# Kernel tuning notes

Hardware: AMD Instinct MI355X
Metric: run time of the kernel (lower is better)

## Reference

```python
import jax, jax.numpy as jnp
from jax import lax
import numpy as np

IN_CH, OUT_CH, K, STRIDE = 4, 256, 16, 8
D_STATE, D_CONV, EXPAND, HEADDIM = 128, 4, 2, 64
D_INNER = EXPAND * OUT_CH            # 512
NHEADS = D_INNER // HEADDIM          # 8
CONV_DIM = D_INNER + 2 * D_STATE     # 768 (ngroups=1)
D_IN_PROJ = 2 * D_INNER + 2 * D_STATE + NHEADS  # 1288
B_SZ, L = 8, 16384


def _conv1d(x, w, b, stride, padding):
    y = lax.conv_general_dilated(x, w, (stride,), padding,
                                 dimension_numbers=('NCH', 'OIH', 'NCH'))
    return y + b[None, :, None]


def _mamba2(u, in_proj_w, conv1d_w, conv1d_b, dt_bias, A_log, D_skip, norm_w, out_proj_w):
    # u: (b, l, d_model). Faithful Mamba2 forward (ngroups=1, rmsnorm gated, no biases on projections).
    b, l, _ = u.shape
    zxbcdt = jnp.einsum('bld,ed->ble', u, in_proj_w)           # (b, l, d_in_proj)
    z = zxbcdt[..., :D_INNER]
    xBC = zxbcdt[..., D_INNER:D_INNER + CONV_DIM]
    dt = jax.nn.softplus(zxbcdt[..., D_INNER + CONV_DIM:] + dt_bias)  # (b, l, h)
    # causal depthwise conv (torch pads d_conv-1 both sides then truncates to :l == left-pad only) + SiLU
    xBC = lax.conv_general_dilated(xBC.transpose(0, 2, 1), conv1d_w, (1,),
                                   [(D_CONV - 1, 0)], feature_group_count=CONV_DIM,
                                   dimension_numbers=('NCH', 'OIH', 'NCH'))
    xBC = jax.nn.silu((xBC + conv1d_b[None, :, None]).transpose(0, 2, 1))  # (b, l, conv_dim)
    xs = xBC[..., :D_INNER].reshape(b, l, NHEADS, HEADDIM)
    Bm = xBC[..., D_INNER:D_INNER + D_STATE]                   # (b, l, n)
    Cm = xBC[..., D_INNER + D_STATE:]                          # (b, l, n)
    A = -jnp.exp(A_log)                                        # (h,), scalar A per head
    dA = jnp.exp(dt * A)                                       # (b, l, h)

    def step(h, inp):
        dA_t, dt_t, x_t, B_t, C_t = inp
        h = h * dA_t[:, :, None, None] + jnp.einsum('bh,bhp,bn->bhpn', dt_t, x_t, B_t)
        return h, jnp.einsum('bhpn,bn->bhp', h, C_t)

    h0 = jnp.zeros((b, NHEADS, HEADDIM, D_STATE), dtype=u.dtype)
    _, ys = lax.scan(step, h0, (dA.swapaxes(0, 1), dt.swapaxes(0, 1),
                                xs.swapaxes(0, 1), Bm.swapaxes(0, 1), Cm.swapaxes(0, 1)))
    y = ys.swapaxes(0, 1) + D_skip[None, None, :, None] * xs   # (b, l, h, p)
    y = y.reshape(b, l, D_INNER) * jax.nn.silu(z)              # gated RMSNorm (norm_before_gate=False)
    y = y * lax.rsqrt(jnp.mean(y * y, axis=-1, keepdims=True) + 1e-5) * norm_w
    return jnp.einsum('ble,de->bld', y, out_proj_w)


def _forward(x, conv_w, conv_b, in_proj_w, conv1d_w, conv1d_b, dt_bias, A_log,
             D_skip, norm_w, out_proj_w, conv1_w, conv1_b, convT_w, convT_b):
    h = jax.nn.relu(_conv1d(x, conv_w, conv_b, STRIDE, 'VALID'))       # (b, out_ch, l')
    y = _mamba2(h.transpose(0, 2, 1), in_proj_w, conv1d_w, conv1d_b,
                dt_bias, A_log, D_skip, norm_w, out_proj_w)
    y = y.transpose(0, 2, 1)                                           # (b, out_ch, l')
    y = _conv1d(y, conv1_w, conv1_b, 1, [(7, 8)])  # torch padding='same', even kernel: left=7, right=8
    # ConvTranspose1d: torch weight (Cin, Cout, K) -> flipped OIH kernel + lhs dilation
    kern = jnp.flip(convT_w, -1).transpose(1, 0, 2)
    y = lax.conv_general_dilated(y, kern, (1,), [(K - 1, K - 1)], lhs_dilation=(STRIDE,),
                                 dimension_numbers=('NCH', 'OIH', 'NCH'))
    return y + convT_b[None, :, None]


def setup_inputs() -> dict:
    key = jax.random.key(0)
    ks = jax.random.split(key, 16)
    n = lambda k, shp, sc=0.05: jax.random.normal(k, shp, dtype=jnp.float32) * sc
    return {
        'x': jax.random.normal(ks[0], (B_SZ, IN_CH, L), dtype=jnp.float32),
        'conv_w': n(ks[1], (OUT_CH, IN_CH, K)),
        'conv_b': n(ks[2], (OUT_CH,)),
        'in_proj_w': n(ks[3], (D_IN_PROJ, OUT_CH)),
        'conv1d_w': n(ks[4], (CONV_DIM, 1, D_CONV), 0.3),
        'conv1d_b': n(ks[5], (CONV_DIM,), 0.1),
        'dt_bias': n(ks[6], (NHEADS,), 0.5),
        'A_log': jnp.log(jax.random.uniform(ks[7], (NHEADS,), minval=1.0, maxval=16.0)),
        'D_skip': n(ks[8], (NHEADS,), 1.0),
        'norm_w': jnp.ones((D_INNER,), dtype=jnp.float32),
        'out_proj_w': n(ks[9], (OUT_CH, D_INNER)),
        'conv1_w': n(ks[10], (STRIDE, OUT_CH, K)),
        'conv1_b': n(ks[11], (STRIDE,)),
        'convT_w': n(ks[12], (STRIDE, IN_CH, K)),
        'convT_b': n(ks[13], (IN_CH,)),
    }


def reference(x, conv_w, conv_b, in_proj_w, conv1d_w, conv1d_b, dt_bias, A_log,
              D_skip, norm_w, out_proj_w, conv1_w, conv1_b, convT_w, convT_b):
    return _forward(x, conv_w, conv_b, in_proj_w, conv1d_w, conv1d_b, dt_bias, A_log,
                    D_skip, norm_w, out_proj_w, conv1_w, conv1_b, convT_w, convT_b)
```

## Files before the change

### kernel.cpp

```cpp
#include <hip/hip_runtime.h>
#include <cstddef>
#include <cstdint>

constexpr int L_IN   = 16384;
constexpr int L_SEQ  = 2047;
constexpr int BATCH  = 8;
constexpr int M_TOK  = BATCH * L_SEQ;
constexpr int D_INNER = 512;
constexpr int NHEADS  = 8;
constexpr int HEADDIM = 64;
constexpr int D_STATE = 128;
constexpr int CONV_DIM = 768;
constexpr int D_IN_PROJ = 1288;

constexpr int QC  = 64;
constexpr int NCH = 32;

constexpr size_t OFF_U    = 0;
constexpr size_t OFF_PB   = OFF_U   + 2096128;
constexpr size_t OFF_ZB   = OFF_U   + 4192256;
constexpr size_t OFF_XBC  = OFF_ZB  + 4192256;
constexpr size_t OFF_DT   = OFF_XBC + 6288384;
constexpr size_t OFF_AW   = OFF_DT  + 131008;
constexpr size_t OFF_XC   = OFF_AW  + 131008;
constexpr size_t OFF_Y    = OFF_XC  + 6288384;
constexpr size_t OFF_YC1  = OFF_Y   + 4192256;
constexpr size_t OFF_PBUF = OFF_YC1 + 131008;
constexpr size_t OFF_HS   = OFF_PBUF + 2048;
constexpr size_t OFF_WBIN = OFF_HS  + 8388608;
constexpr size_t OFF_WBF  = OFF_WBIN + 164864;
constexpr size_t OFF_W2   = OFF_WBF + 8192;

using short8 = __attribute__((ext_vector_type(8))) short;
using f32x4  = __attribute__((ext_vector_type(4))) float;
typedef unsigned short ushort_t;

__device__ __forceinline__ ushort_t f2bf(float f) {
  uint32_t u = __float_as_uint(f);
  u += 0x7fffu + ((u >> 16) & 1u);
  return (ushort_t)(u >> 16);
}
__device__ __forceinline__ float bf2f(ushort_t h) {
  return __uint_as_float(((uint32_t)h) << 16);
}
__device__ __forceinline__ float siluf(float a) { return a / (1.f + expf(-a)); }
#define MFMA16(a, b, c) __builtin_amdgcn_mfma_f32_16x16x32_bf16(a, b, c, 0, 0, 0)

#define GLD_LDS(gp, lp) __builtin_amdgcn_global_load_lds( \
    (const __attribute__((address_space(1))) void*)(gp),  \
    (__attribute__((address_space(3))) void*)(lp), 16, 0, 0)

__global__ __launch_bounds__(256) void k_prep(const float* __restrict__ x,
    const float* __restrict__ w1, const float* __restrict__ w3,
    const float* __restrict__ conv1_w, const float* __restrict__ wout,
    ushort_t* __restrict__ PB, ushort_t* __restrict__ o1, ushort_t* __restrict__ o3,
    ushort_t* __restrict__ W2b) {
  const int bid = blockIdx.x;
  const int tid = threadIdx.x;
  if (bid < 512) {
    int idx = bid * 256 + tid;
    if (idx >= M_TOK * 8) return;
    int oct = idx & 7, row = idx >> 3;
    int t = row % L_SEQ, b = row / L_SEQ;
    int ic = oct >> 1, k0 = (oct & 1) * 8;
    const float* src = x + ((size_t)b * 4 + ic) * L_IN + t * 8 + k0;
    float4 a0 = *(const float4*)src;
    float4 a1 = *(const float4*)(src + 4);
    short8 o;
    o[0] = (short)f2bf(a0.x); o[1] = (short)f2bf(a0.y);
    o[2] = (short)f2bf(a0.z); o[3] = (short)f2bf(a0.w);
    o[4] = (short)f2bf(a1.x); o[5] = (short)f2bf(a1.y);
    o[6] = (short)f2bf(a1.z); o[7] = (short)f2bf(a1.w);
    *(short8*)(PB + (size_t)row * 64 + oct * 8) = o;
  } else if (bid < 1800) {
    int i = (bid - 512) * 256 + tid;
    if (i < D_IN_PROJ * 256) o1[i] = f2bf(w1[i]);
    if (i < 256 * 64)        o3[i] = f2bf(w3[i]);
  } else {
    const int r = bid - 1800;
    const int oc = r >> 4, k = r & 15;
    const int d0 = tid;
    float acc0 = 0.f, acc1 = 0.f;
    for (int o = 0; o < 256; o++) {
      float wv = conv1_w[((size_t)oc * 256 + o) * 16 + k];
      acc0 = fmaf(wv, wout[(size_t)o * 512 + d0], acc0);
      acc1 = fmaf(wv, wout[(size_t)o * 512 + d0 + 256], acc1);
    }
    W2b[(size_t)r * 512 + d0]       = f2bf(acc0);
    W2b[(size_t)r * 512 + d0 + 256] = f2bf(acc1);
  }
}

template<int EPI>
__global__ __launch_bounds__(256) void gemm_bf16(const ushort_t* __restrict__ A, int lda,
    const ushort_t* __restrict__ B, int ldb, float* __restrict__ C,
    const float* __restrict__ bias, int M, int N, int K, int nx,
    ushort_t* __restrict__ zb, ushort_t* __restrict__ xbcb,
    float* __restrict__ dtb, float* __restrict__ awb,
    const float* __restrict__ dt_bias, const float* __restrict__ A_log) {
  __shared__ __attribute__((aligned(16))) ushort_t sA[2][128 * 64];
  __shared__ __attribute__((aligned(16))) ushort_t sB[2][128 * 64];
  const int tid = threadIdx.x;
  const int cpx = gridDim.x >> 3;
  const int swz = (blockIdx.x & 7) * cpx + (blockIdx.x >> 3);
  const int m0 = (swz / nx) * 128, n0 = (swz % nx) * 128;
  const int w = tid >> 6, lane = tid & 63;
  const int l15 = lane & 15, lK = lane >> 4;
  const int wr = w >> 1, wc = w & 1;
  f32x4 acc[4][4] = {};

  auto STAGE = [&](int buf, int k0) {
#pragma unroll
    for (int j = 0; j < 4; j++) {
      int idx = j * 256 + tid;
      int r = idx >> 3;
      int ss = (idx & 7) ^ (r & 7);
      GLD_LDS(A + (size_t)(m0 + r) * lda + k0 + ss * 8, &sA[buf][(j * 256 + w * 64) * 8]);
      GLD_LDS(B + (size_t)(n0 + r) * ldb + k0 + ss * 8, &sB[buf][(j * 256 + w * 64) * 8]);
    }
  };

  STAGE(0, 0);
  __syncthreads();
  int cur = 0;
  for (int k0 = 0; k0 < K; k0 += 64) {
    if (k0 + 64 < K) STAGE(cur ^ 1, k0 + 64);
#pragma unroll
    for (int kk = 0; kk < 2; kk++) {
      short8 af[4], bf[4];
#pragma unroll
      for (int mt = 0; mt < 4; mt++) {
        int r = wr * 64 + mt * 16 + l15;
        af[mt] = *(const short8*)&sA[cur][r * 64 + (((kk * 4 + lK) ^ (r & 7)) * 8)];
      }
#pragma unroll
      for (int nt = 0; nt < 4; nt++) {
        int r = wc * 64 + nt * 16 + l15;
        bf[nt] = *(const short8*)&sB[cur][r * 64 + (((kk * 4 + lK) ^ (r & 7)) * 8)];
      }
#pragma unroll
      for (int mt = 0; mt < 4; mt++)
#pragma unroll
        for (int nt = 0; nt < 4; nt++)
          acc[mt][nt] = MFMA16(af[mt], bf[nt], acc[mt][nt]);
    }
    __syncthreads();
    cur ^= 1;
  }
  if constexpr (EPI == 0) {
#pragma unroll
    for (int mt = 0; mt < 4; mt++)
#pragma unroll
      for (int i = 0; i < 4; i++) {
        int gm = m0 + wr * 64 + mt * 16 + lK * 4 + i;
        if (gm < M) {
          float* crow = C + (size_t)gm * N;
#pragma unroll
          for (int nt = 0; nt < 4; nt++) {
            int gn = n0 + wc * 64 + nt * 16 + l15;
            if (gn < N) crow[gn] = acc[mt][nt][i];
          }
        }
      }
  } else if constexpr (EPI == 1) {
    ushort_t* Cb = (ushort_t*)C;
#pragma unroll
    for (int mt = 0; mt < 4; mt++)
#pragma unroll
      for (int i = 0; i < 4; i++) {
        int gm = m0 + wr * 64 + mt * 16 + lK * 4 + i;
#pragma unroll
        for (int nt = 0; nt < 4; nt++) {
          int gn = n0 + wc * 64 + nt * 16 + l15;
          float v = fmaxf(acc[mt][nt][i] + bias[gn], 0.f);
          uint32_t mine = f2bf(v);
          uint32_t other = (uint32_t)__shfl_xor((int)mine, 1, 64);
          if (((lane & 1) == 0) && gm < M)
            *(uint32_t*)(Cb + (size_t)gm * N + gn) = mine | (other << 16);
        }
      }
  } else {
    if (n0 < 1280) {
      ushort_t* dst = (n0 < 512) ? zb : xbcb;
      const int ldd  = (n0 < 512) ? 512 : 768;
      const int coff = (n0 < 512) ? 0 : 512;
#pragma unroll
      for (int mt = 0; mt < 4; mt++)
#pragma unroll
        for (int i = 0; i < 4; i++) {
          int gm = m0 + wr * 64 + mt * 16 + lK * 4 + i;
#pragma unroll
          for (int nt = 0; nt < 4; nt++) {
            int gn = n0 + wc * 64 + nt * 16 + l15;
            uint32_t mine = f2bf(acc[mt][nt][i]);
            uint32_t other = (uint32_t)__shfl_xor((int)mine, 1, 64);
            if (((lane & 1) == 0) && gm < M)
              *(uint32_t*)(dst + (size_t)gm * ldd + (gn - coff)) = mine | (other << 16);
          }
        }
    } else {
#pragma unroll
      for (int mt = 0; mt < 4; mt++)
#pragma unroll
        for (int i = 0; i < 4; i++) {
          int gm = m0 + wr * 64 + mt * 16 + lK * 4 + i;
          if (gm >= M) continue;
#pragma unroll
          for (int nt = 0; nt < 4; nt++) {
            int gn = n0 + wc * 64 + nt * 16 + l15;
            if (gn < N) {
              int hd = gn - 1280;
              float v = acc[mt][nt][i] + dt_bias[hd];
              float sp = (v > 20.f) ? v : log1pf(expf(v));
              dtb[(size_t)gm * 8 + hd] = sp;
              awb[(size_t)gm * 8 + hd] = -expf(A_log[hd]) * sp;
            }
          }
        }
    }
  }
}

__global__ __launch_bounds__(192) void k_dw(const ushort_t* __restrict__ xbcb,
    const float* __restrict__ w, const float* __restrict__ bias,
    ushort_t* __restrict__ xcb) {
  const int bid = blockIdx.x;
  const int tb = bid & 511, b = bid >> 9;
  const int t0 = tb * 4;
  const int c = threadIdx.x * 4;
  const size_t rowb = (size_t)b * L_SEQ;
  float wr[4][4];
#pragma unroll
  for (int j = 0; j < 4; j++)
#pragma unroll
    for (int k = 0; k < 4; k++) wr[j][k] = w[(c + j) * 4 + k];
  const float4 bs = {bias[c], bias[c + 1], bias[c + 2], bias[c + 3]};
  float v[7][4];
#pragma unroll
  for (int r = 0; r < 7; r++) {
    int tt = t0 - 3 + r;
    if (tt >= 0 && tt < L_SEQ) {
      uint2 pk = *(const uint2*)(xbcb + (rowb + tt) * CONV_DIM + c);
      v[r][0] = bf2f((ushort_t)(pk.x & 0xffff));
      v[r][1] = bf2f((ushort_t)(pk.x >> 16));
      v[r][2] = bf2f((ushort_t)(pk.y & 0xffff));
      v[r][3] = bf2f((ushort_t)(pk.y >> 16));
    } else {
      v[r][0] = v[r][1] = v[r][2] = v[r][3] = 0.f;
    }
  }
#pragma unroll
  for (int o = 0; o < 4; o++) {
    int t = t0 + o;
    if (t >= L_SEQ) break;
    float a0 = bs.x, a1 = bs.y, a2 = bs.z, a3 = bs.w;
#pragma unroll
    for (int k = 0; k < 4; k++) {
      a0 = fmaf(v[o + k][0], wr[0][k], a0);
      a1 = fmaf(v[o + k][1], wr[1][k], a1);
      a2 = fmaf(v[o + k][2], wr[2][k], a2);
      a3 = fmaf(v[o + k][3], wr[3][k], a3);
    }
    uint2 ov;
    ov.x = (uint32_t)f2bf(siluf(a0)) | ((uint32_t)f2bf(siluf(a1)) << 16);
    ov.y = (uint32_t)f2bf(siluf(a2)) | ((uint32_t)f2bf(siluf(a3)) << 16);
    *(uint2*)(xcb + (rowb + t) * CONV_DIM + c) = ov;
  }
}

__global__ __launch_bounds__(256) void k_ssd_state(const ushort_t* __restrict__ xcb,
    const float* __restrict__ dtb, const float* __restrict__ aw,
    ushort_t* __restrict__ HSb, float* __restrict__ Pbuf) {
  const int ch = blockIdx.x, bh = blockIdx.y;
  const int b = bh >> 3, h = bh & 7;
  const int t0 = ch * QC;
  const int valid = (L_SEQ - t0 < QC) ? (L_SEQ - t0) : QC;
  const size_t rowbase = (size_t)b * L_SEQ;
  __shared__ __attribute__((aligned(16))) short sBT[128][72];
  __shared__ __attribute__((aligned(16))) short sXw[64][72];
  __shared__ float sW[64];
  __shared__ float sLtot;
  const int tid = threadIdx.x;
  if (tid < 64) {
    float aa = 0.f, dd = 0.f;
    if (tid < valid) { size_t r8 = (rowbase + t0 + tid) * 8 + h; aa = aw[r8]; dd = dtb[r8]; }
    float s = aa;
#pragma unroll
    for (int d = 1; d < 64; d <<= 1) { float o = __shfl_up(s, d, 64); if (tid >= d) s += o; }
    float Lt = __shfl(s, 63, 64);
    sW[tid] = expf(Lt - s) * dd;
    if (tid == 63) sLtot = s;
  }
  __syncthreads();
  for (int i = tid; i < 64 * 16; i += 256) {
    int r = i >> 4, q = (i & 15) * 8;
    short8 v = {0, 0, 0, 0, 0, 0, 0, 0};
    if (r < valid) v = *(const short8*)(xcb + (rowbase + t0 + r) * CONV_DIM + 512 + q);
#pragma unroll
    for (int j = 0; j < 8; j++) sBT[q + j][r] = v[j];
  }
  for (int i = tid; i < 64 * 8; i += 256) {
    int r = i >> 3, q = (i & 7) * 8;
    short8 v = {0, 0, 0, 0, 0, 0, 0, 0};
    if (r < valid) v = *(const short8*)(xcb + (rowbase + t0 + r) * CONV_DIM + h * 64 + q);
    float wv = sW[r];
#pragma unroll
    for (int j = 0; j < 8; j++) sXw[q + j][r] = (short)f2bf(bf2f((ushort_t)v[j]) * wv);
  }
  __syncthreads();
  const int w = tid >> 6, l15 = tid & 15, lK = (tid & 63) >> 4;
  f32x4 acc[2][4] = {};
  short8 afr[2][2];
#pragma unroll
  for (int j = 0; j < 2; j++)
#pragma unroll
    for (int kt = 0; kt < 2; kt++)
      afr[j][kt] = *(const short8*)&sBT[(w * 2 + j) * 16 + l15][kt * 32 + lK * 8];
#pragma unroll
  for (int pt = 0; pt < 4; pt++) {
#pragma unroll
    for (int kt = 0; kt < 2; kt++) {
      short8 bfr = *(const short8*)&sXw[pt * 16 + l15][kt * 32 + lK * 8];
      acc[0][pt] = MFMA16(afr[0][kt], bfr, acc[0][pt]);
      acc[1][pt] = MFMA16(afr[1][kt], bfr, acc[1][pt]);
    }
  }
  ushort_t* dst = HSb + ((size_t)bh * NCH + ch) * 8192;
#pragma unroll
  for (int j = 0; j < 2; j++)
#pragma unroll
    for (int pt = 0; pt < 4; pt++)
#pragma unroll
      for (int i = 0; i < 4; i++) {
        int n = (w * 2 + j) * 16 + lK * 4 + i, p = pt * 16 + l15;
        uint32_t mine = f2bf(acc[j][pt][i]);
        uint32_t other = (uint32_t)__shfl_xor((int)mine, 1, 64);
        if ((l15 & 1) == 0)
          *(uint32_t*)(dst + n * 64 + p) = mine | (other << 16);
      }
  if (tid == 0) Pbuf[bh * NCH + ch] = expf(sLtot);
}

__global__ __launch_bounds__(256) void k_ssd_comb(ushort_t* __restrict__ HSb,
                                                  const float* __restrict__ Pbuf) {
  const int bh = blockIdx.y;
  const int e2 = blockIdx.x * 256 + threadIdx.x;
  const size_t base = (size_t)bh * NCH * 8192 + (size_t)e2 * 2;
  uint32_t pk[NCH];
  float P[NCH];
#pragma unroll
  for (int c = 0; c < NCH; c++) pk[c] = *(const uint32_t*)(HSb + base + (size_t)c * 8192);
#pragma unroll
  for (int c = 0; c < NCH; c++) P[c] = Pbuf[bh * NCH + c];
  float run0 = 0.f, run1 = 0.f;
#pragma unroll
  for (int c = 0; c < NCH; c++) {
    run0 = fmaf(P[c], run0, bf2f((ushort_t)(pk[c] & 0xffff)));
    run1 = fmaf(P[c], run1, bf2f((ushort_t)(pk[c] >> 16)));
    pk[c] = (uint32_t)f2bf(run0) | ((uint32_t)f2bf(run1) << 16);
  }
#pragma unroll
  for (int c = 0; c < NCH; c++) *(uint32_t*)(HSb + base + (size_t)c * 8192) = pk[c];
}

__global__ __launch_bounds__(256) void k_ssd_y(const ushort_t* __restrict__ xcb,
    const float* __restrict__ dtb, const float* __restrict__ aw,
    const float* __restrict__ Dskip, const ushort_t* __restrict__ HSb,
    ushort_t* __restrict__ y16) {
  const int ch = blockIdx.x, bh = blockIdx.y;
  const int b = bh >> 3, h = bh & 7;
  const int t0 = ch * QC;
  const int valid = (L_SEQ - t0 < QC) ? (L_SEQ - t0) : QC;
  const size_t rowbase = (size_t)b * L_SEQ;
  __shared__ __attribute__((aligned(16))) short sB[64][136];
  __shared__ __attribute__((aligned(16))) short sC[64][136];
  __shared__ __attribute__((aligned(16))) short sH[64][136];
  __shared__ __attribute__((aligned(16))) short sX[64][72];
  __shared__ float sLrel[64], sdt[64], sEL[64];
  short (*sM)[72] = (short(*)[72])&sB[0][0];
  const int tid = threadIdx.x;
  if (tid < 64) {
    float aa = 0.f, dd = 0.f;
    if (tid < valid) { size_t r8 = (rowbase + t0 + tid) * 8 + h; aa = aw[r8]; dd = dtb[r8]; }
    float s = aa;
#pragma unroll
    for (int d = 1; d < 64; d <<= 1) { float o = __shfl_up(s, d, 64); if (tid >= d) s += o; }
    sLrel[tid] = s; sdt[tid] = dd; sEL[tid] = expf(s);
  }
  for (int i = tid; i < 64 * 16; i += 256) {
    int r = i >> 4, q = (i & 15) * 8;
    short8 vb = {0, 0, 0, 0, 0, 0, 0, 0}, vc = {0, 0, 0, 0, 0, 0, 0, 0};
    if (r < valid) {
      const ushort_t* rp = xcb + (rowbase + t0 + r) * CONV_DIM;
      vb = *(const short8*)(rp + 512 + q);
      vc = *(const short8*)(rp + 640 + q);
    }
#pragma unroll
    for (int j = 0; j < 8; j++) { sB[r][q + j] = vb[j]; sC[r][q + j] = vc[j]; }
  }
  for (int i = tid; i < 64 * 8; i += 256) {
    int r = i >> 3, q = (i & 7) * 8;
    short8 v = {0, 0, 0, 0, 0, 0, 0, 0};
    if (r < valid) v = *(const short8*)(xcb + (rowbase + t0 + r) * CONV_DIM + h * 64 + q);
#pragma unroll
    for (int j = 0; j < 8; j++) sX[q + j][r] = v[j];
  }
  for (int i = tid; i < 128 * 8; i += 256) {
    int n = i >> 3, q = (i & 7) * 8;
    short8 v = {0, 0, 0, 0, 0, 0, 0, 0};
    if (ch > 0) v = *(const short8*)(HSb + ((size_t)bh * NCH + (ch - 1)) * 8192 + n * 64 + q);
#pragma unroll
    for (int j = 0; j < 8; j++) sH[q + j][n] = v[j];
  }
  __syncthreads();
  const int w = tid >> 6, l15 = tid & 15, lK = (tid & 63) >> 4;
  short8 aC[4];
#pragma unroll
  for (int kt = 0; kt < 4; kt++)
    aC[kt] = *(const short8*)&sC[w * 16 + l15][kt * 32 + lK * 8];
  f32x4 g[4] = {};
#pragma unroll
  for (int st = 0; st < 4; st++)
#pragma unroll
    for (int kt = 0; kt < 4; kt++)
      g[st] = MFMA16(aC[kt], *(const short8*)&sB[st * 16 + l15][kt * 32 + lK * 8], g[st]);
  __syncthreads();
#pragma unroll
  for (int st = 0; st < 4; st++)
#pragma unroll
    for (int i = 0; i < 4; i++) {
      int tt = w * 16 + lK * 4 + i, ss = st * 16 + l15;
      float f = (ss <= tt) ? expf(sLrel[tt] - sLrel[ss]) * sdt[ss] : 0.f;
      sM[tt][ss] = (short)f2bf(g[st][i] * f);
    }
  __syncthreads();
  f32x4 acc[4] = {};
#pragma unroll
  for (int pt = 0; pt < 4; pt++)
#pragma unroll
    for (int kt = 0; kt < 4; kt++)
      acc[pt] = MFMA16(aC[kt], *(const short8*)&sH[pt * 16 + l15][kt * 32 + lK * 8], acc[pt]);
#pragma unroll
  for (int pt = 0; pt < 4; pt++)
#pragma unroll
    for (int i = 0; i < 4; i++)
      acc[pt][i] *= sEL[w * 16 + lK * 4 + i];
  short8 aM[2];
#pragma unroll
  for (int kt = 0; kt < 2; kt++)
    aM[kt] = *(const short8*)&sM[w * 16 + l15][kt * 32 + lK * 8];
#pragma unroll
  for (int pt = 0; pt < 4; pt++)
#pragma unroll
    for (int kt = 0; kt < 2; kt++)
      acc[pt] = MFMA16(aM[kt], *(const short8*)&sX[pt * 16 + l15][kt * 32 + lK * 8], acc[pt]);
  const float Dsk = Dskip[h];
#pragma unroll
  for (int pt = 0; pt < 4; pt++)
#pragma unroll
    for (int i = 0; i < 4; i++) {
      int tt = w * 16 + lK * 4 + i;
      int pp = pt * 16 + l15;
      float v = acc[pt][i] + Dsk * bf2f((ushort_t)sX[pp][tt]);
      uint32_t mine = f2bf(v);
      uint32_t other = (uint32_t)__shfl_xor((int)mine, 1, 64);
      if (((l15 & 1) == 0) && tt < valid)
        *(uint32_t*)(y16 + (rowbase + t0 + tt) * D_INNER + h * 64 + pp) = mine | (other << 16);
    }
}

__global__ __launch_bounds__(256) void k_norm(ushort_t* __restrict__ y16,
    const ushort_t* __restrict__ zb, const float* __restrict__ norm_w) {
  const int row = blockIdx.x * 4 + (threadIdx.x >> 6);
  const int lane = threadIdx.x & 63;
  const int c0 = lane * 8;
  ushort_t* yrow = y16 + (size_t)row * D_INNER;
  short8 yv = *(const short8*)(yrow + c0);
  short8 zv = *(const short8*)(zb + (size_t)row * 512 + c0);
  float v[8];
  float ss = 0.f;
#pragma unroll
  for (int j = 0; j < 8; j++) {
    float z = bf2f((ushort_t)zv[j]);
    float g = z / (1.f + expf(-z));
    v[j] = bf2f((ushort_t)yv[j]) * g;
    ss += v[j] * v[j];
  }
#pragma unroll
  for (int m = 32; m >= 1; m >>= 1) ss += __shfl_xor(ss, m, 64);
  float scale = rsqrtf(ss * (1.f / 512.f) + 1e-5f);
  float4 nw0 = *(const float4*)(norm_w + c0);
  float4 nw1 = *(const float4*)(norm_w + c0 + 4);
  short8 o;
  o[0] = (short)f2bf(v[0] * scale * nw0.x); o[1] = (short)f2bf(v[1] * scale * nw0.y);
  o[2] = (short)f2bf(v[2] * scale * nw0.z); o[3] = (short)f2bf(v[3] * scale * nw0.w);
  o[4] = (short)f2bf(v[4] * scale * nw1.x); o[5] = (short)f2bf(v[5] * scale * nw1.y);
  o[6] = (short)f2bf(v[6] * scale * nw1.z); o[7] = (short)f2bf(v[7] * scale * nw1.w);
  *(short8*)(yrow + c0) = o;
}

__global__ __launch_bounds__(256) void k_tail(const float* __restrict__ Yg,
    const float* __restrict__ b1, const float* __restrict__ wT,
    const float* __restrict__ bT, float* __restrict__ out) {
  const int bid = blockIdx.x;
  const int sc = bid & 31, b = bid >> 5;
  const int s0 = sc * 512;
  const int mbase = (s0 - 15) >> 3;
  const int tid = threadIdx.x;
  __shared__ float sY[8][66];
  __shared__ float swT[8][4][16];
  __shared__ float sb1[8], sbT[4];
  for (int i = tid; i < 512; i += 256) {
    int j = i >> 6, c = (i >> 4) & 3, k = i & 15;
    swT[j][c][k] = wT[((size_t)j * 4 + c) * 16 + k];
  }
  if (tid < 8) sb1[tid] = b1[tid];
  if (tid < 4) sbT[tid] = bT[tid];
  __syncthreads();
  const float* Yb = Yg + (size_t)b * L_SEQ * 128;
  for (int item = tid; item < 8 * 66; item += 256) {
    int j = item / 66, ii = item % 66;
    int m = mbase + ii;
    float acc = 0.f;
    if ((unsigned)m < (unsigned)L_SEQ) {
      acc = sb1[j];
#pragma unroll
      for (int k = 0; k < 16; k++) {
        int tt = m - 7 + k;
        if ((unsigned)tt < (unsigned)L_SEQ) acc += Yb[(size_t)tt * 128 + j * 16 + k];
      }
    }
    sY[j][ii] = acc;
  }
  __syncthreads();
  const int c = tid >> 6, si = tid & 63;
  float ov[8];
#pragma unroll
  for (int u = 0; u < 8; u++) {
    int s = s0 + si * 8 + u;
    float acc = sbT[c];
    const int k0 = (15 - u) & 7;
#pragma unroll
    for (int dk = 0; dk < 2; dk++) {
      int k = k0 + 8 * dk;
      int num = s - 15 + k;
      int m = num >> 3;
      if (num >= 0 && m < L_SEQ) {
        int ii = m - mbase;
#pragma unroll
        for (int j = 0; j < 8; j++)
          acc = fmaf(sY[j][ii], swT[j][c][15 - k], acc);
      }
    }
    ov[u] = acc;
  }
  float* op = out + ((size_t)b * 4 + c) * L_IN + s0 + si * 8;
  *(float4*)op       = *(float4*)&ov[0];
  *(float4*)(op + 4) = *(float4*)&ov[4];
}

extern "C" void kernel_launch(void* const* d_in, const int* in_sizes, int n_in,
                              void* d_out, int out_size, void* d_ws, size_t ws_size,
                              hipStream_t stream) {
  const float* x         = (const float*)d_in[0];
  const float* conv_w    = (const float*)d_in[1];
  const float* conv_b    = (const float*)d_in[2];
  const float* in_proj_w = (const float*)d_in[3];
  const float* conv1d_w  = (const float*)d_in[4];
  const float* conv1d_b  = (const float*)d_in[5];
  const float* dt_bias   = (const float*)d_in[6];
  const float* A_log     = (const float*)d_in[7];
  const float* D_skip    = (const float*)d_in[8];
  const float* norm_w    = (const float*)d_in[9];
  const float* out_proj_w= (const float*)d_in[10];
  const float* conv1_w   = (const float*)d_in[11];
  const float* conv1_b   = (const float*)d_in[12];
  const float* convT_w   = (const float*)d_in[13];
  const float* convT_b   = (const float*)d_in[14];
  float* out = (float*)d_out;
  float* ws  = (float*)d_ws;

  ushort_t* ub   = (ushort_t*)(ws + OFF_U);
  ushort_t* PB   = (ushort_t*)(ws + OFF_PB);
  ushort_t* zb   = (ushort_t*)(ws + OFF_ZB);
  ushort_t* xbcb = (ushort_t*)(ws + OFF_XBC);
  float* dtb  = ws + OFF_DT;
  float* awb  = ws + OFF_AW;
  ushort_t* xcb = (ushort_t*)(ws + OFF_XC);
  ushort_t* y16 = (ushort_t*)(ws + OFF_Y);
  float* Pbuf = ws + OFF_PBUF;
  ushort_t* HSb = (ushort_t*)(ws + OFF_HS);
  ushort_t* wbin  = (ushort_t*)(ws + OFF_WBIN);
  ushort_t* wbf   = (ushort_t*)(ws + OFF_WBF);
  ushort_t* W2b   = (ushort_t*)(ws + OFF_W2);
  float* Yg   = ws + OFF_U;

  k_prep<<<dim3(1928), 256, 0, stream>>>(x, in_proj_w, conv_w, conv1_w, out_proj_w,
                                         PB, wbin, wbf, W2b);
  gemm_bf16<1><<<dim3(256), 256, 0, stream>>>(PB, 64, wbf, 64, (float*)ub,
      conv_b, M_TOK, 256, 64, 2, nullptr, nullptr, nullptr, nullptr, nullptr, nullptr);
  gemm_bf16<2><<<dim3(1408), 256, 0, stream>>>(ub, 256, wbin, 256, nullptr,
      nullptr, M_TOK, D_IN_PROJ, 256, 11, zb, xbcb, dtb, awb, dt_bias, A_log);
  k_dw<<<dim3(BATCH * 512), 192, 0, stream>>>(xbcb, conv1d_w, conv1d_b, xcb);
  k_ssd_state<<<dim3(NCH, 64), 256, 0, stream>>>(xcb, dtb, awb, HSb, Pbuf);
  k_ssd_comb<<<dim3(16, 64), 256, 0, stream>>>(HSb, Pbuf);
  k_ssd_y<<<dim3(NCH, 64), 256, 0, stream>>>(xcb, dtb, awb, D_skip, HSb, y16);
  k_norm<<<dim3(M_TOK / 4), 256, 0, stream>>>(y16, zb, norm_w);
  gemm_bf16<0><<<dim3(128), 256, 0, stream>>>(y16, 512, W2b, 512, Yg,
      nullptr, M_TOK, 128, D_INNER, 1, nullptr, nullptr, nullptr, nullptr, nullptr, nullptr);
  k_tail<<<dim3(256), 256, 0, stream>>>(Yg, conv1_b, convT_w, convT_b, out);
}
```

Before: 198.7 us.

## Fuse x-channel depthwise conv into SSD kernels and single-buffer GEMM LDS

The depthwise causal conv+SiLU for the 512 x channels is now computed on the fly inside k_ssd_state and k_ssd_y from the raw xBC buffer, while k_dw only processes the B/C channels into a compact 256-wide buffer. This cuts the write and reread of the x part of the conv output. In exchange each SSD kernel recomputes the conv and reads four overlapping input rows per token. Separately, the GEMM drops LDS double buffering for a single buffer with two barriers per K step, which lowers LDS use (possibly raising occupancy) but removes load/compute overlap.

```diff
diff --git a/kernel.cpp b/kernel.cpp
--- a/kernel.cpp
+++ b/kernel.cpp
@@ -98,8 +98,8 @@
     ushort_t* __restrict__ zb, ushort_t* __restrict__ xbcb,
     float* __restrict__ dtb, float* __restrict__ awb,
     const float* __restrict__ dt_bias, const float* __restrict__ A_log) {
-  __shared__ __attribute__((aligned(16))) ushort_t sA[2][128 * 64];
-  __shared__ __attribute__((aligned(16))) ushort_t sB[2][128 * 64];
+  __shared__ __attribute__((aligned(16))) ushort_t sA[128 * 64];
+  __shared__ __attribute__((aligned(16))) ushort_t sB[128 * 64];
   const int tid = threadIdx.x;
   const int cpx = gridDim.x >> 3;
   const int swz = (blockIdx.x & 7) * cpx + (blockIdx.x >> 3);
@@ -108,35 +108,29 @@
   const int l15 = lane & 15, lK = lane >> 4;
   const int wr = w >> 1, wc = w & 1;
   f32x4 acc[4][4] = {};
-
-  auto STAGE = [&](int buf, int k0) {
+  for (int k0 = 0; k0 < K; k0 += 64) {
+    __syncthreads();
 #pragma unroll
     for (int j = 0; j < 4; j++) {
       int idx = j * 256 + tid;
       int r = idx >> 3;
       int ss = (idx & 7) ^ (r & 7);
-      GLD_LDS(A + (size_t)(m0 + r) * lda + k0 + ss * 8, &sA[buf][(j * 256 + w * 64) * 8]);
-      GLD_LDS(B + (size_t)(n0 + r) * ldb + k0 + ss * 8, &sB[buf][(j * 256 + w * 64) * 8]);
-    }
-  };
-
-  STAGE(0, 0);
-  __syncthreads();
-  int cur = 0;
-  for (int k0 = 0; k0 < K; k0 += 64) {
-    if (k0 + 64 < K) STAGE(cur ^ 1, k0 + 64);
+      GLD_LDS(A + (size_t)(m0 + r) * lda + k0 + ss * 8, &sA[(j * 256 + w * 64) * 8]);
+      GLD_LDS(B + (size_t)(n0 + r) * ldb + k0 + ss * 8, &sB[(j * 256 + w * 64) * 8]);
+    }
+    __syncthreads();
 #pragma unroll
     for (int kk = 0; kk < 2; kk++) {
       short8 af[4], bf[4];
 #pragma unroll
       for (int mt = 0; mt < 4; mt++) {
         int r = wr * 64 + mt * 16 + l15;
-        af[mt] = *(const short8*)&sA[cur][r * 64 + (((kk * 4 + lK) ^ (r & 7)) * 8)];
+        af[mt] = *(const short8*)&sA[r * 64 + (((kk * 4 + lK) ^ (r & 7)) * 8)];
       }
 #pragma unroll
       for (int nt = 0; nt < 4; nt++) {
         int r = wc * 64 + nt * 16 + l15;
-        bf[nt] = *(const short8*)&sB[cur][r * 64 + (((kk * 4 + lK) ^ (r & 7)) * 8)];
+        bf[nt] = *(const short8*)&sB[r * 64 + (((kk * 4 + lK) ^ (r & 7)) * 8)];
       }
 #pragma unroll
       for (int mt = 0; mt < 4; mt++)
@@ -144,8 +138,6 @@
         for (int nt = 0; nt < 4; nt++)
           acc[mt][nt] = MFMA16(af[mt], bf[nt], acc[mt][nt]);
     }
-    __syncthreads();
-    cur ^= 1;
   }
   if constexpr (EPI == 0) {
 #pragma unroll
@@ -221,7 +213,7 @@
   }
 }
 
-__global__ __launch_bounds__(192) void k_dw(const ushort_t* __restrict__ xbcb,
+__global__ __launch_bounds__(64) void k_dw(const ushort_t* __restrict__ xbcb,
     const float* __restrict__ w, const float* __restrict__ bias,
     ushort_t* __restrict__ xcb) {
   const int bid = blockIdx.x;
@@ -233,14 +225,14 @@
 #pragma unroll
   for (int j = 0; j < 4; j++)
 #pragma unroll
-    for (int k = 0; k < 4; k++) wr[j][k] = w[(c + j) * 4 + k];
-  const float4 bs = {bias[c], bias[c + 1], bias[c + 2], bias[c + 3]};
+    for (int k = 0; k < 4; k++) wr[j][k] = w[(512 + c + j) * 4 + k];
+  const float4 bs = {bias[512 + c], bias[512 + c + 1], bias[512 + c + 2], bias[512 + c + 3]};
   float v[7][4];
 #pragma unroll
   for (int r = 0; r < 7; r++) {
     int tt = t0 - 3 + r;
     if (tt >= 0 && tt < L_SEQ) {
-      uint2 pk = *(const uint2*)(xbcb + (rowb + tt) * CONV_DIM + c);
+      uint2 pk = *(const uint2*)(xbcb + (rowb + tt) * CONV_DIM + 512 + c);
       v[r][0] = bf2f((ushort_t)(pk.x & 0xffff));
       v[r][1] = bf2f((ushort_t)(pk.x >> 16));
       v[r][2] = bf2f((ushort_t)(pk.y & 0xffff));
@@ -264,11 +256,13 @@
     uint2 ov;
     ov.x = (uint32_t)f2bf(siluf(a0)) | ((uint32_t)f2bf(siluf(a1)) << 16);
     ov.y = (uint32_t)f2bf(siluf(a2)) | ((uint32_t)f2bf(siluf(a3)) << 16);
-    *(uint2*)(xcb + (rowb + t) * CONV_DIM + c) = ov;
+    *(uint2*)(xcb + (rowb + t) * 256 + c) = ov;
   }
 }
 
 __global__ __launch_bounds__(256) void k_ssd_state(const ushort_t* __restrict__ xcb,
+    const ushort_t* __restrict__ xbcb, const float* __restrict__ cw,
+    const float* __restrict__ cb,
     const float* __restrict__ dtb, const float* __restrict__ aw,
     ushort_t* __restrict__ HSb, float* __restrict__ Pbuf) {
   const int ch = blockIdx.x, bh = blockIdx.y;
@@ -295,17 +289,44 @@
   for (int i = tid; i < 64 * 16; i += 256) {
     int r = i >> 4, q = (i & 15) * 8;
     short8 v = {0, 0, 0, 0, 0, 0, 0, 0};
-    if (r < valid) v = *(const short8*)(xcb + (rowbase + t0 + r) * CONV_DIM + 512 + q);
+    if (r < valid) v = *(const short8*)(xcb + (rowbase + t0 + r) * 256 + q);
 #pragma unroll
     for (int j = 0; j < 8; j++) sBT[q + j][r] = v[j];
   }
-  for (int i = tid; i < 64 * 8; i += 256) {
-    int r = i >> 3, q = (i & 7) * 8;
-    short8 v = {0, 0, 0, 0, 0, 0, 0, 0};
-    if (r < valid) v = *(const short8*)(xcb + (rowbase + t0 + r) * CONV_DIM + h * 64 + q);
-    float wv = sW[r];
-#pragma unroll
-    for (int j = 0; j < 8; j++) sXw[q + j][r] = (short)f2bf(bf2f((ushort_t)v[j]) * wv);
+  {
+    const int q = (tid & 7) * 8;
+    float4 w4[8]; float b8[8];
+#pragma unroll
+    for (int j = 0; j < 8; j++) {
+      w4[j] = *(const float4*)(cw + (size_t)(h * 64 + q + j) * 4);
+      b8[j] = cb[h * 64 + q + j];
+    }
+    for (int i = tid; i < 64 * 8; i += 256) {
+      int r = i >> 3;
+      if (r < valid) {
+        float a[8];
+#pragma unroll
+        for (int j = 0; j < 8; j++) a[j] = b8[j];
+#pragma unroll
+        for (int k = 0; k < 4; k++) {
+          int tt = t0 + r - 3 + k;
+          if (tt >= 0) {
+            short8 v = *(const short8*)(xbcb + (rowbase + tt) * CONV_DIM + h * 64 + q);
+#pragma unroll
+            for (int j = 0; j < 8; j++) {
+              float wk = (k == 0) ? w4[j].x : (k == 1) ? w4[j].y : (k == 2) ? w4[j].z : w4[j].w;
+              a[j] = fmaf(bf2f((ushort_t)v[j]), wk, a[j]);
+            }
+          }
+        }
+        float wv = sW[r];
+#pragma unroll
+        for (int j = 0; j < 8; j++) sXw[q + j][r] = (short)f2bf(siluf(a[j]) * wv);
+      } else {
+#pragma unroll
+        for (int j = 0; j < 8; j++) sXw[q + j][r] = 0;
+      }
+    }
   }
   __syncthreads();
   const int w = tid >> 6, l15 = tid & 15, lK = (tid & 63) >> 4;
@@ -364,6 +385,8 @@
 }
 
 __global__ __launch_bounds__(256) void k_ssd_y(const ushort_t* __restrict__ xcb,
+    const ushort_t* __restrict__ xbcb, const float* __restrict__ cw,
+    const float* __restrict__ cb,
     const float* __restrict__ dtb, const float* __restrict__ aw,
     const float* __restrict__ Dskip, const ushort_t* __restrict__ HSb,
     ushort_t* __restrict__ y16) {
@@ -391,19 +414,46 @@
     int r = i >> 4, q = (i & 15) * 8;
     short8 vb = {0, 0, 0, 0, 0, 0, 0, 0}, vc = {0, 0, 0, 0, 0, 0, 0, 0};
     if (r < valid) {
-      const ushort_t* rp = xcb + (rowbase + t0 + r) * CONV_DIM;
-      vb = *(const short8*)(rp + 512 + q);
-      vc = *(const short8*)(rp + 640 + q);
+      const ushort_t* rp = xcb + (rowbase + t0 + r) * 256;
+      vb = *(const short8*)(rp + q);
+      vc = *(const short8*)(rp + 128 + q);
     }
 #pragma unroll
     for (int j = 0; j < 8; j++) { sB[r][q + j] = vb[j]; sC[r][q + j] = vc[j]; }
   }
-  for (int i = tid; i < 64 * 8; i += 256) {
-    int r = i >> 3, q = (i & 7) * 8;
-    short8 v = {0, 0, 0, 0, 0, 0, 0, 0};
-    if (r < valid) v = *(const short8*)(xcb + (rowbase + t0 + r) * CONV_DIM + h * 64 + q);
-#pragma unroll
-    for (int j = 0; j < 8; j++) sX[q + j][r] = v[j];
+  {
+    const int q = (tid & 7) * 8;
+    float4 w4[8]; float b8[8];
+#pragma unroll
+    for (int j = 0; j < 8; j++) {
+      w4[j] = *(const float4*)(cw + (size_t)(h * 64 + q + j) * 4);
+      b8[j] = cb[h * 64 + q + j];
+    }
+    for (int i = tid; i < 64 * 8; i += 256) {
+      int r = i >> 3;
+      if (r < valid) {
+        float a[8];
+#pragma unroll
+        for (int j = 0; j < 8; j++) a[j] = b8[j];
+#pragma unroll
+        for (int k = 0; k < 4; k++) {
+          int tt = t0 + r - 3 + k;
+          if (tt >= 0) {
+            short8 v = *(const short8*)(xbcb + (rowbase + tt) * CONV_DIM + h * 64 + q);
+#pragma unroll
+            for (int j = 0; j < 8; j++) {
+              float wk = (k == 0) ? w4[j].x : (k == 1) ? w4[j].y : (k == 2) ? w4[j].z : w4[j].w;
+              a[j] = fmaf(bf2f((ushort_t)v[j]), wk, a[j]);
+            }
+          }
+        }
+#pragma unroll
+        for (int j = 0; j < 8; j++) sX[q + j][r] = (short)f2bf(siluf(a[j]));
+      } else {
+#pragma unroll
+        for (int j = 0; j < 8; j++) sX[q + j][r] = 0;
+      }
+    }
   }
   for (int i = tid; i < 128 * 8; i += 256) {
     int n = i >> 3, q = (i & 7) * 8;
@@ -601,10 +651,12 @@
       conv_b, M_TOK, 256, 64, 2, nullptr, nullptr, nullptr, nullptr, nullptr, nullptr);
   gemm_bf16<2><<<dim3(1408), 256, 0, stream>>>(ub, 256, wbin, 256, nullptr,
       nullptr, M_TOK, D_IN_PROJ, 256, 11, zb, xbcb, dtb, awb, dt_bias, A_log);
-  k_dw<<<dim3(BATCH * 512), 192, 0, stream>>>(xbcb, conv1d_w, conv1d_b, xcb);
-  k_ssd_state<<<dim3(NCH, 64), 256, 0, stream>>>(xcb, dtb, awb, HSb, Pbuf);
+  k_dw<<<dim3(BATCH * 512), 64, 0, stream>>>(xbcb, conv1d_w, conv1d_b, xcb);
+  k_ssd_state<<<dim3(NCH, 64), 256, 0, stream>>>(xcb, xbcb, conv1d_w, conv1d_b,
+                                                 dtb, awb, HSb, Pbuf);
   k_ssd_comb<<<dim3(16, 64), 256, 0, stream>>>(HSb, Pbuf);
-  k_ssd_y<<<dim3(NCH, 64), 256, 0, stream>>>(xcb, dtb, awb, D_skip, HSb, y16);
+  k_ssd_y<<<dim3(NCH, 64), 256, 0, stream>>>(xcb, xbcb, conv1d_w, conv1d_b,
+                                             dtb, awb, D_skip, HSb, y16);
   k_norm<<<dim3(M_TOK / 4), 256, 0, stream>>>(y16, zb, norm_w);
   gemm_bf16<0><<<dim3(128), 256, 0, stream>>>(y16, 512, W2b, 512, Yg,
       nullptr, M_TOK, 128, D_INNER, 1, nullptr, nullptr, nullptr, nullptr, nullptr, nullptr);
```

New measurement: 214.7 us. 1.08x slower.
